# Kernel optimization log

Measured on AMD Instinct MI355X. Metric: run time of the kernel, lower is better.

## Reference

```python
import jax, jax.numpy as jnp
import numpy as np

DIM = 192
HEADS = 6
HEAD_DIM = DIM // HEADS
WS = 8            # window size
N = WS * WS       # tokens per window
IN_CC = 16        # top-k kept keys per query
B, H, W = 8, 64, 64
NEG = -100.0      # value used by the torch code for masked logits
EPS_NORM = 1e-12  # F.normalize eps
EPS_LN = 1e-5     # nn.LayerNorm eps


def _rel_pos_index(ws):
    coords = np.stack(np.meshgrid(np.arange(ws), np.arange(ws), indexing='ij'))  # (2,ws,ws)
    cf = coords.reshape(2, -1)
    rel = (cf[:, :, None] - cf[:, None, :]).transpose(1, 2, 0).astype(np.int64)  # (N,N,2)
    rel[:, :, 0] += ws - 1
    rel[:, :, 1] += ws - 1
    rel[:, :, 0] *= 2 * ws - 1
    return jnp.asarray(rel.sum(-1))  # (N,N) indices into (2ws-1)^2 table

REL_IDX = _rel_pos_index(WS)


def _layer_norm(x, g, b):
    mu = jnp.mean(x, -1, keepdims=True)
    var = jnp.mean(jnp.square(x - mu), -1, keepdims=True)
    return (x - mu) * jax.lax.rsqrt(var + EPS_LN) * g + b


def _l2n(x):
    n = jnp.sqrt(jnp.sum(jnp.square(x), -1, keepdims=True))
    return x / jnp.maximum(n, EPS_NORM)


def setup_inputs() -> dict:
    key = jax.random.key(0)
    ks = jax.random.split(key, 8)
    s = 0.02
    return {
        'x': jax.random.normal(ks[0], (B, DIM, H, W), jnp.float32),
        'norm1_g': jnp.ones((DIM,), jnp.float32),
        'norm1_b': jnp.zeros((DIM,), jnp.float32),
        'qkv_w': jax.random.normal(ks[1], (3 * DIM, DIM), jnp.float32) * s,
        'qkv_b': jnp.zeros((3 * DIM,), jnp.float32),
        'proj_w': jax.random.normal(ks[2], (DIM, DIM), jnp.float32) * s,
        'proj_b': jnp.zeros((DIM,), jnp.float32),
        'rpb_table': jax.random.normal(ks[3], ((2 * WS - 1) ** 2, HEADS), jnp.float32) * s,
        'temperature': jnp.ones((HEADS, 1, 1), jnp.float32),
        'norm2_g': jnp.ones((DIM,), jnp.float32),
        'norm2_b': jnp.zeros((DIM,), jnp.float32),
        'fc1_w': jax.random.normal(ks[4], (4 * DIM, DIM), jnp.float32) * s,
        'fc1_b': jnp.zeros((4 * DIM,), jnp.float32),
        'fc2_w': jax.random.normal(ks[5], (DIM, 4 * DIM), jnp.float32) * s,
        'fc2_b': jnp.zeros((DIM,), jnp.float32),
    }


def reference(x, norm1_g, norm1_b, qkv_w, qkv_b, proj_w, proj_b, rpb_table,
              temperature, norm2_g, norm2_b, fc1_w, fc1_b, fc2_w, fc2_b):
    b, c, h, w = x.shape
    # (B,C,H,W) -> (B,L,C), pre-norm (note: the torch code norms the shortcut too)
    xs = jnp.transpose(x.reshape(b, c, h * w), (0, 2, 1))
    shortcut = _layer_norm(xs, norm1_g, norm1_b)  # (B,L,C)

    # window partition: (B,H,W,C) -> (B*nWh*nWw, N, C); shift_size=0, no padding (H,W % WS == 0)
    xin = shortcut.reshape(b, h // WS, WS, w // WS, WS, c)
    xin = jnp.transpose(xin, (0, 1, 3, 2, 4, 5)).reshape(-1, N, c)
    B_ = xin.shape[0]

    qkv = (xin @ qkv_w.T + qkv_b).reshape(B_, N, 3, HEADS, HEAD_DIM)
    qkv = jnp.transpose(qkv, (2, 0, 3, 1, 4))  # (3, B_, h, N, d)
    q, k, v = qkv[0], qkv[1], qkv[2]

    # cosine attention with learned per-head temperature
    attn = jnp.einsum('bhnd,bhmd->bhnm', _l2n(q), _l2n(k)) * temperature  # (B_,h,N,N)

    # top-k sparsification: keep IN_CC largest logits per query (threshold == kth value;
    # equivalent to the torch topk+scatter mask for distinct values)
    kth = jax.lax.top_k(attn, IN_CC)[0][..., -1:]
    attn = jnp.where(attn >= kth, attn, NEG)

    # relative position bias gather: (N,N,h) -> (h,N,N)
    rpb = jnp.transpose(rpb_table[REL_IDX], (2, 0, 1))
    attn = jax.nn.softmax(attn + rpb[None], axis=-1)

    out = jnp.einsum('bhnm,bhmd->bhnd', attn, v)
    out = jnp.transpose(out, (0, 2, 1, 3)).reshape(B_, N, c)
    out = out @ proj_w.T + proj_b

    # window reverse -> (B, L, C)
    out = out.reshape(b, h // WS, w // WS, WS, WS, c)
    out = jnp.transpose(out, (0, 1, 3, 2, 4, 5)).reshape(b, h * w, c)

    x2 = shortcut + out  # drop_path = identity (eval)
    hdn = _layer_norm(x2, norm2_g, norm2_b)
    hdn = jax.nn.gelu(hdn @ fc1_w.T + fc1_b, approximate=False) @ fc2_w.T + fc2_b
    x2 = x2 + hdn

    # back to (B,C,H,W)
    return jnp.transpose(x2, (0, 2, 1)).reshape(b, c, h, w)
```

## Files before the change

kernel.cpp:

```cpp
#include <hip/hip_runtime.h>
#include <hip/hip_bf16.h>
#include <math.h>

#define DIM     192
#define HEADS   6
#define HEAD_DIM 32
#define NTOK    64
#define IN_CC   16
#define TTOT    32768
#define NWIN    512

using bf16x8 = __attribute__((ext_vector_type(8))) short;
using f32x4  = __attribute__((ext_vector_type(4))) float;
typedef unsigned short ushort_t;

__device__ __forceinline__ ushort_t f2b(float f) {
    unsigned u = __float_as_uint(f);
    u += 0x7fffu + ((u >> 16) & 1u);
    return (ushort_t)(u >> 16);
}
__device__ __forceinline__ unsigned pk2(float a, float b) {
    return (unsigned)f2b(a) | ((unsigned)f2b(b) << 16);
}
__device__ __forceinline__ float b2f(ushort_t u) {
    return __uint_as_float(((unsigned)u) << 16);
}

__global__ __launch_bounds__(256) void cvt_all_kernel(
    const float* __restrict__ s0, const float* __restrict__ s1,
    const float* __restrict__ s2, const float* __restrict__ s3,
    ushort_t* __restrict__ d0, ushort_t* __restrict__ d1,
    ushort_t* __restrict__ d2, ushort_t* __restrict__ d3)
{
    const int bid = blockIdx.x;
    const float* src; ushort_t* dst; int off, K; bool perm = false;
    if (bid < 108)      { src = s0; dst = d0; off = bid;       K = 192; perm = true; }
    else if (bid < 144) { src = s1; dst = d1; off = bid - 108; K = 192; }
    else if (bid < 288) { src = s2; dst = d2; off = bid - 144; K = 192; }
    else                { src = s3; dst = d3; off = bid - 288; K = 768; }
    const int K8 = K >> 3;
    const int d  = (off * 256 + threadIdx.x) * 4;
    const int frag = d >> 7, win = d & 127;
    const int m16w = win >> 3, k7 = win & 7;
    const int oblk = frag / K8, kblk = frag - oblk * K8;
    const int o = oblk * 16 + m16w, k = kblk * 8 + k7;
    int so = o;
    if (perm && o < 384) {
        const int s = o & 31;
        const int c = (((s >> 2) & 3) << 3) | (((s >> 4) & 1) << 2) | (s & 3);
        so = (o & ~31) | c;
    }
    float4 v = *(const float4*)(src + (size_t)so * K + k);
    ushort4 ov;
    ov.x = f2b(v.x); ov.y = f2b(v.y); ov.z = f2b(v.z); ov.w = f2b(v.w);
    *(ushort4*)(dst + d) = ov;
}

__global__ __launch_bounds__(256) void ln1_kernel(
    const float* __restrict__ x, const float* __restrict__ g,
    const float* __restrict__ bb, ushort_t* __restrict__ outh)
{
    __shared__ float xs[64][193];
    __shared__ float mu_s[64], rs_s[64];
    __shared__ float gs[192], bs[192];
    const int tid = threadIdx.x;
    const int t0  = blockIdx.x * 64;
    const int b   = t0 >> 12;
    const int hw0 = t0 & 4095;
    if (tid < 192) { gs[tid] = g[tid]; bs[tid] = bb[tid]; }
    const int tok = tid & 63, qq = tid >> 6;
    const float* xb = x + (size_t)b * (DIM * 4096) + hw0 + tok;
    #pragma unroll
    for (int it = 0; it < 48; ++it) {
        int c = it * 4 + qq;
        xs[tok][c] = xb[(size_t)c * 4096];
    }
    __syncthreads();
    const int tok2 = tid >> 2, p = tid & 3;
    float sum = 0.f;
    #pragma unroll
    for (int c = 0; c < 48; ++c) sum += xs[tok2][p * 48 + c];
    sum += __shfl_xor(sum, 1);
    sum += __shfl_xor(sum, 2);
    const float m = sum * (1.0f / 192.0f);
    float ss = 0.f;
    #pragma unroll
    for (int c = 0; c < 48; ++c) { float d = xs[tok2][p * 48 + c] - m; ss += d * d; }
    ss += __shfl_xor(ss, 1);
    ss += __shfl_xor(ss, 2);
    if (p == 0) {
        mu_s[tok2] = m;
        rs_s[tok2] = 1.0f / sqrtf(ss * (1.0f / 192.0f) + 1e-5f);
    }
    __syncthreads();
    ushort_t* obh = outh + (size_t)t0 * DIM;
    #pragma unroll
    for (int it = 0; it < 48; ++it) {
        int idx = it * 256 + tid;
        int tk = idx / 192, c = idx % 192;
        obh[idx] = f2b((xs[tk][c] - mu_s[tk]) * rs_s[tk] * gs[c] + bs[c]);
    }
}

__global__ __launch_bounds__(384, 3) void attn_fused(
    const ushort_t* __restrict__ sc_h, const ushort_t* __restrict__ wqf,
    const float* __restrict__ qkv_b, const float* __restrict__ rpb_table,
    const float* __restrict__ temp, const ushort_t* __restrict__ wpf,
    const float* __restrict__ proj_b, float* __restrict__ x2)
{
    __shared__ __align__(16) char smem[63840];
    const int tid  = threadIdx.x;
    const int wave = tid >> 6, n = tid & 63;
    char* arena = smem + wave * 9728;
    float*    Ssq = (float*)arena;
    ushort_t* Ph  = (ushort_t*)arena;
    ushort_t* Vt  = (ushort_t*)(arena + 4608);
    float*    ksb = (float*)(arena + 9216);
    float*    qnb = (float*)(arena + 9472);
    float*    rpb = (float*)(smem + 58368) + wave * 228;
    ushort_t (*AoT)[200] = (ushort_t(*)[200])smem;
    float* Cwj = (float*)(smem + 25600 + wave * 5120);

    const int win = blockIdx.x;
    const int h   = wave;
    const int b   = win >> 6;
    const int wh  = (win >> 3) & 7, ww = win & 7;
    const int i1  = n >> 3, j1 = n & 7;
    const int m16 = n & 15, quad = n >> 4;

    for (int r = n; r < 225; r += 64) rpb[r] = rpb_table[r * 6 + h];

    int trow[4];
    #pragma unroll
    for (int i = 0; i < 4; ++i) {
        const int row = 16 * i + m16;
        trow[i] = b * 4096 + (wh * 8 + (row >> 3)) * 64 + ww * 8 + (row & 7);
    }

    bf16x8 qA[4], kB[4];
    #pragma unroll
    for (int part = 0; part < 3; ++part) {
        const int o0 = part * 192 + h * 32;
        f32x4 pa[4][2];
        #pragma unroll
        for (int i = 0; i < 4; ++i)
            #pragma unroll
            for (int j = 0; j < 2; ++j)
                pa[i][j] = (f32x4)(0.0f);
        const ushort_t* Wb = wqf + (size_t)(o0 >> 4) * 24 * 128 + m16 * 8;
        for (int ks = 0; ks < 192; ks += 32) {
            bf16x8 af[4], wv[2];
            #pragma unroll
            for (int i = 0; i < 4; ++i)
                af[i] = *(const bf16x8*)(sc_h + (size_t)trow[i] * 192 + ks + quad * 8);
            #pragma unroll
            for (int j = 0; j < 2; ++j)
                wv[j] = *(const bf16x8*)(Wb + (size_t)(j * 24 + (ks >> 3) + quad) * 128);
            #pragma unroll
            for (int i = 0; i < 4; ++i)
                #pragma unroll
                for (int j = 0; j < 2; ++j)
                    pa[i][j] = __builtin_amdgcn_mfma_f32_16x16x32_bf16(wv[j], af[i], pa[i][j], 0, 0, 0);
        }
        if (part < 2) {
            const float4 bv0 = *(const float4*)&qkv_b[o0 + 8 * quad];
            const float4 bv1 = *(const float4*)&qkv_b[o0 + 8 * quad + 4];
            float ssq[4];
            #pragma unroll
            for (int i = 0; i < 4; ++i) {
                f32x4 v0 = pa[i][0], v1 = pa[i][1];
                v0[0] += bv0.x; v0[1] += bv0.y; v0[2] += bv0.z; v0[3] += bv0.w;
                v1[0] += bv1.x; v1[1] += bv1.y; v1[2] += bv1.z; v1[3] += bv1.w;
                float sq = 0.f;
                #pragma unroll
                for (int r = 0; r < 4; ++r) sq += v0[r] * v0[r] + v1[r] * v1[r];
                ssq[i] = sq;
                bf16x8 fr;
                fr[0] = (short)f2b(v0[0]); fr[1] = (short)f2b(v0[1]);
                fr[2] = (short)f2b(v0[2]); fr[3] = (short)f2b(v0[3]);
                fr[4] = (short)f2b(v1[0]); fr[5] = (short)f2b(v1[1]);
                fr[6] = (short)f2b(v1[2]); fr[7] = (short)f2b(v1[3]);
                if (part == 0) qA[i] = fr; else kB[i] = fr;
            }
            #pragma unroll
            for (int i = 0; i < 4; ++i) {
                ssq[i] += __shfl_xor(ssq[i], 16);
                ssq[i] += __shfl_xor(ssq[i], 32);
            }
            if (quad == 0) {
                #pragma unroll
                for (int i = 0; i < 4; ++i) {
                    if (part == 0) qnb[16 * i + m16] = ssq[i];
                    else           ksb[4 * m16 + i]  = 1.0f / fmaxf(sqrtf(ssq[i]), 1e-12f);
                }
            }
        } else {
            const float4 bv0 = *(const float4*)&qkv_b[o0 + quad * 4];
            const float4 bv1 = *(const float4*)&qkv_b[o0 + 16 + quad * 4];
            #pragma unroll
            for (int i = 0; i < 4; ++i) {
                f32x4 v0 = pa[i][0], v1 = pa[i][1];
                v0[0] += bv0.x; v0[1] += bv0.y; v0[2] += bv0.z; v0[3] += bv0.w;
                v1[0] += bv1.x; v1[1] += bv1.y; v1[2] += bv1.z; v1[3] += bv1.w;
                #pragma unroll
                for (int r = 0; r < 4; ++r) {
                    Vt[(quad * 4 + r) * 72 + 4 * m16 + i]      = f2b(v0[r]);
                    Vt[(16 + quad * 4 + r) * 72 + 4 * m16 + i] = f2b(v1[r]);
                }
            }
        }
    }

    f32x4 acc[4][4];
    #pragma unroll
    for (int i = 0; i < 4; ++i)
        #pragma unroll
        for (int j = 0; j < 4; ++j)
            acc[i][j] = __builtin_amdgcn_mfma_f32_16x16x32_bf16(qA[i], kB[j], (f32x4)(0.0f), 0, 0, 0);

    float s[64];
    #pragma unroll
    for (int i = 0; i < 4; ++i) {
        #pragma unroll
        for (int r = 0; r < 4; ++r) {
            f32x4 vv = { acc[i][0][r], acc[i][1][r], acc[i][2][r], acc[i][3][r] };
            *(f32x4*)&Ssq[(4 * quad + r) * 68 + 4 * m16] = vv;
        }
        if ((n >> 4) == i) {
            #pragma unroll
            for (int c = 0; c < 16; ++c)
                *(float4*)&s[4 * c] = *(const float4*)&Ssq[(n & 15) * 68 + 4 * c];
        }
    }

    const float qs = temp[h] / fmaxf(sqrtf(qnb[n]), 1e-12f);
    #pragma unroll
    for (int c = 0; c < 16; ++c) {
        float4 kv = *(const float4*)&ksb[4 * c];
        s[4*c+0] *= qs * kv.x; s[4*c+1] *= qs * kv.y;
        s[4*c+2] *= qs * kv.z; s[4*c+3] *= qs * kv.w;
    }

    float thr = 1e30f;
    for (int it = 0; it < IN_CC; ++it) {
        float mx = -1e30f;
        #pragma unroll
        for (int m = 0; m < 64; ++m) {
            float vv = (s[m] < thr) ? s[m] : -1e30f;
            mx = fmaxf(mx, vv);
        }
        thr = mx;
    }

    const int basen = i1 * 15 + j1;
    float mx = -1e30f;
    #pragma unroll
    for (int c = 0; c < 64; ++c) {
        const int m = 16 * (c & 3) + (c >> 2);
        const int i2 = m >> 3, j2 = m & 7;
        float vv = ((s[c] >= thr) ? s[c] : -100.0f)
                 + rpb[basen + (7 - i2) * 15 + (7 - j2)];
        s[c] = vv;
        mx = fmaxf(mx, vv);
    }
    float sum = 0.f;
    #pragma unroll
    for (int c = 0; c < 64; ++c) { float e = __expf(s[c] - mx); s[c] = e; sum += e; }
    const float inv = 1.0f / sum;
    #pragma unroll
    for (int c = 0; c < 64; ++c) s[c] *= inv;

    bf16x8 vb[2][2];
    #pragma unroll
    for (int kh2 = 0; kh2 < 2; ++kh2)
        #pragma unroll
        for (int j2 = 0; j2 < 2; ++j2)
            vb[kh2][j2] = *(const bf16x8*)&Vt[(16 * j2 + m16) * 72 + kh2 * 32 + quad * 8];

    f32x4 o[4][2];
    #pragma unroll
    for (int i = 0; i < 4; ++i)
        #pragma unroll
        for (int j2 = 0; j2 < 2; ++j2)
            o[i][j2] = (f32x4)(0.0f);
    #pragma unroll
    for (int hf = 0; hf < 2; ++hf) {
        if ((n >> 5) == hf) {
            #pragma unroll
            for (int g = 0; g < 8; ++g) {
                uint4 w;
                w.x = pk2(s[8*g+0], s[8*g+1]); w.y = pk2(s[8*g+2], s[8*g+3]);
                w.z = pk2(s[8*g+4], s[8*g+5]); w.w = pk2(s[8*g+6], s[8*g+7]);
                *(uint4*)&Ph[(n & 31) * 72 + 8 * g] = w;
            }
        }
        #pragma unroll
        for (int ih = 0; ih < 2; ++ih) {
            const int i = 2 * hf + ih;
            #pragma unroll
            for (int kh2 = 0; kh2 < 2; ++kh2) {
                bf16x8 pafr = *(const bf16x8*)&Ph[(16 * ih + m16) * 72 + kh2 * 32 + quad * 8];
                o[i][0] = __builtin_amdgcn_mfma_f32_16x16x32_bf16(pafr, vb[kh2][0], o[i][0], 0, 0, 0);
                o[i][1] = __builtin_amdgcn_mfma_f32_16x16x32_bf16(pafr, vb[kh2][1], o[i][1], 0, 0, 0);
            }
        }
    }
    __syncthreads();

    #pragma unroll
    for (int i = 0; i < 4; ++i) {
        #pragma unroll
        for (int r = 0; r < 4; ++r) {
            const int row = 16 * i + 4 * quad + r;
            AoT[row][h * 32 + m16]      = f2b(o[i][0][r]);
            AoT[row][h * 32 + 16 + m16] = f2b(o[i][1][r]);
        }
    }
    __syncthreads();

    f32x4 pacc[4][2];
    #pragma unroll
    for (int i = 0; i < 4; ++i)
        #pragma unroll
        for (int j = 0; j < 2; ++j)
            pacc[i][j] = (f32x4)(0.0f);
    const ushort_t* Wb = wpf + (size_t)(wave * 2) * 24 * 128 + m16 * 8;
    for (int ks = 0; ks < 192; ks += 32) {
        bf16x8 af[4], wv[2];
        #pragma unroll
        for (int i = 0; i < 4; ++i)
            af[i] = *(const bf16x8*)&AoT[16 * i + m16][quad * 8 + ks];
        #pragma unroll
        for (int j = 0; j < 2; ++j)
            wv[j] = *(const bf16x8*)(Wb + (size_t)(j * 24 + (ks >> 3) + quad) * 128);
        #pragma unroll
        for (int i = 0; i < 4; ++i)
            #pragma unroll
            for (int j = 0; j < 2; ++j)
                pacc[i][j] = __builtin_amdgcn_mfma_f32_16x16x32_bf16(wv[j], af[i], pacc[i][j], 0, 0, 0);
    }

    #pragma unroll
    for (int j = 0; j < 2; ++j) {
        const float4 bj = *(const float4*)&proj_b[wave * 32 + 16 * j + quad * 4];
        #pragma unroll
        for (int i = 0; i < 4; ++i) {
            f32x4 v = pacc[i][j];
            v[0] += bj.x; v[1] += bj.y; v[2] += bj.z; v[3] += bj.w;
            *(f32x4*)&Cwj[(16 * i + m16) * 20 + quad * 4] = v;
        }
        #pragma unroll
        for (int q = 0; q < 4; ++q) {
            const int idx = q * 64 + n;
            const int row = idx >> 2, c4 = (idx & 3) * 4;
            const int ii = row >> 3, jj = row & 7;
            const int tt = b * 4096 + (wh * 8 + ii) * 64 + ww * 8 + jj;
            const int oc = wave * 32 + 16 * j + c4;
            float4 vv = *(const float4*)&Cwj[row * 20 + c4];
            uint2 rv = *(const uint2*)&sc_h[(size_t)tt * 192 + oc];
            vv.x += b2f((ushort_t)(rv.x & 0xffffu));
            vv.y += b2f((ushort_t)(rv.x >> 16));
            vv.z += b2f((ushort_t)(rv.y & 0xffffu));
            vv.w += b2f((ushort_t)(rv.y >> 16));
            *(float4*)&x2[(size_t)tt * DIM + oc] = vv;
        }
    }
}

__global__ __launch_bounds__(256) void mlp_fused(
    const float* __restrict__ x2, const ushort_t* __restrict__ w1f,
    const ushort_t* __restrict__ w2f, const float* __restrict__ fc1_b,
    const float* __restrict__ fc2_b, const float* __restrict__ g2,
    const float* __restrict__ b2, float* __restrict__ outp)
{
    __shared__ __align__(16) char smem[43008];
    ushort_t (*h_h)[200] = (ushort_t(*)[200])smem;
    ushort_t (*a1c)[136] = (ushort_t(*)[136])(smem + 25600);
    float* gs  = (float*)(smem + 25600);
    float* bs  = gs + 192;

    const int tid  = threadIdx.x;
    const int wave = tid >> 6, lane = tid & 63;
    const int m16 = lane & 15, quad = lane >> 4;
    const int t0 = blockIdx.x * 64;
    const int b   = t0 >> 12;
    const int hw0 = t0 & 4095;

    if (tid < 192) { gs[tid] = g2[tid]; bs[tid] = b2[tid]; }
    __syncthreads();
    {
        const int tok = tid >> 2, p = tid & 3;
        const float* rp = x2 + (size_t)(t0 + tok) * DIM + p * 48;
        float xv[48];
        #pragma unroll
        for (int c4 = 0; c4 < 12; ++c4)
            *(float4*)&xv[c4 * 4] = *(const float4*)(rp + c4 * 4);
        float sum = 0.f;
        #pragma unroll
        for (int c = 0; c < 48; ++c) sum += xv[c];
        sum += __shfl_xor(sum, 1);
        sum += __shfl_xor(sum, 2);
        const float m = sum * (1.0f / 192.0f);
        float ss = 0.f;
        #pragma unroll
        for (int c = 0; c < 48; ++c) { float d = xv[c] - m; ss += d * d; }
        ss += __shfl_xor(ss, 1);
        ss += __shfl_xor(ss, 2);
        const float rs = 1.0f / sqrtf(ss * (1.0f / 192.0f) + 1e-5f);
        ushort_t* hp = &h_h[tok][p * 48];
        #pragma unroll
        for (int c2 = 0; c2 < 24; ++c2) {
            float v0 = (xv[2*c2]   - m) * rs * gs[p * 48 + 2*c2]   + bs[p * 48 + 2*c2];
            float v1 = (xv[2*c2+1] - m) * rs * gs[p * 48 + 2*c2+1] + bs[p * 48 + 2*c2+1];
            *(unsigned*)(hp + 2 * c2) = pk2(v0, v1);
        }
    }
    __syncthreads();

    f32x4 acc2[4][3];
    #pragma unroll
    for (int i = 0; i < 4; ++i)
        #pragma unroll
        for (int j = 0; j < 3; ++j)
            acc2[i][j] = (f32x4)(0.0f);

    for (int c = 0; c < 6; ++c) {
        f32x4 acc1[4][2];
        #pragma unroll
        for (int i = 0; i < 4; ++i)
            #pragma unroll
            for (int j = 0; j < 2; ++j)
                acc1[i][j] = (f32x4)(0.0f);
        const ushort_t* Wb1 = w1f + (size_t)(c * 8 + wave * 2) * 24 * 128 + m16 * 8;
        for (int ks = 0; ks < 192; ks += 32) {
            bf16x8 af[4], wv[2];
            #pragma unroll
            for (int i = 0; i < 4; ++i)
                af[i] = *(const bf16x8*)&h_h[16 * i + m16][quad * 8 + ks];
            #pragma unroll
            for (int j = 0; j < 2; ++j)
                wv[j] = *(const bf16x8*)(Wb1 + (size_t)(j * 24 + (ks >> 3) + quad) * 128);
            #pragma unroll
            for (int i = 0; i < 4; ++i)
                #pragma unroll
                for (int j = 0; j < 2; ++j)
                    acc1[i][j] = __builtin_amdgcn_mfma_f32_16x16x32_bf16(wv[j], af[i], acc1[i][j], 0, 0, 0);
        }
        #pragma unroll
        for (int j = 0; j < 2; ++j) {
            const int o = c * 128 + wave * 32 + 16 * j + quad * 4;
            const float4 bv = *(const float4*)&fc1_b[o];
            #pragma unroll
            for (int i = 0; i < 4; ++i) {
                f32x4 v = acc1[i][j];
                v[0] += bv.x; v[1] += bv.y; v[2] += bv.z; v[3] += bv.w;
                #pragma unroll
                for (int r = 0; r < 4; ++r) {
                    float xg = v[r];
                    float e1 = __expf(xg * (1.5957691f + 0.0713548f * xg * xg)) + 1.0f;
                    v[r] = xg - xg * __builtin_amdgcn_rcpf(e1);
                }
                uint2 pkd;
                pkd.x = pk2(v[0], v[1]); pkd.y = pk2(v[2], v[3]);
                *(uint2*)&a1c[16 * i + m16][wave * 32 + 16 * j + quad * 4] = pkd;
            }
        }
        __syncthreads();
        const ushort_t* Wb2 = w2f + (size_t)(wave * 3) * 96 * 128 + m16 * 8;
        for (int ks = 0; ks < 128; ks += 32) {
            bf16x8 af2[4], wv2[3];
            #pragma unroll
            for (int i = 0; i < 4; ++i)
                af2[i] = *(const bf16x8*)&a1c[16 * i + m16][quad * 8 + ks];
            #pragma unroll
            for (int j = 0; j < 3; ++j)
                wv2[j] = *(const bf16x8*)(Wb2 + (size_t)(j * 96 + c * 16 + (ks >> 3) + quad) * 128);
            #pragma unroll
            for (int i = 0; i < 4; ++i)
                #pragma unroll
                for (int j = 0; j < 3; ++j)
                    acc2[i][j] = __builtin_amdgcn_mfma_f32_16x16x32_bf16(wv2[j], af2[i], acc2[i][j], 0, 0, 0);
        }
        __syncthreads();
    }

    float (*Cw)[68] = (float(*)[68])(smem + wave * 8704);
    float4 b2j[3];
    #pragma unroll
    for (int j = 0; j < 3; ++j)
        b2j[j] = *(const float4*)&fc2_b[wave * 48 + 16 * j + quad * 4];
    #pragma unroll
    for (int p = 0; p < 2; ++p) {
        #pragma unroll
        for (int ih = 0; ih < 2; ++ih) {
            const int i = 2 * p + ih;
            #pragma unroll
            for (int j = 0; j < 3; ++j) {
                f32x4 v = acc2[i][j];
                v[0] += b2j[j].x; v[1] += b2j[j].y; v[2] += b2j[j].z; v[3] += b2j[j].w;
                *(f32x4*)&Cw[ih * 16 + m16][16 * j + quad * 4] = v;
            }
        }
        #pragma unroll
        for (int q = 0; q < 6; ++q) {
            const int idx = q * 64 + lane;
            const int cc = idx >> 3, t4 = (idx & 7) * 4;
            const int o  = wave * 48 + cc;
            const int tb = t0 + p * 32 + t4;
            float4 vv;
            vv.x = Cw[t4 + 0][cc] + x2[(size_t)(tb + 0) * DIM + o];
            vv.y = Cw[t4 + 1][cc] + x2[(size_t)(tb + 1) * DIM + o];
            vv.z = Cw[t4 + 2][cc] + x2[(size_t)(tb + 2) * DIM + o];
            vv.w = Cw[t4 + 3][cc] + x2[(size_t)(tb + 3) * DIM + o];
            *(float4*)&outp[(size_t)b * (DIM * 4096) + (size_t)o * 4096
                            + hw0 + p * 32 + t4] = vv;
        }
    }
}

extern "C" void kernel_launch(void* const* d_in, const int* in_sizes, int n_in,
                              void* d_out, int out_size, void* d_ws, size_t ws_size,
                              hipStream_t stream)
{
    const float* x        = (const float*)d_in[0];
    const float* norm1_g  = (const float*)d_in[1];
    const float* norm1_b  = (const float*)d_in[2];
    const float* qkv_w    = (const float*)d_in[3];
    const float* qkv_b    = (const float*)d_in[4];
    const float* proj_w   = (const float*)d_in[5];
    const float* proj_b   = (const float*)d_in[6];
    const float* rpbt     = (const float*)d_in[7];
    const float* temp     = (const float*)d_in[8];
    const float* norm2_g  = (const float*)d_in[9];
    const float* norm2_b  = (const float*)d_in[10];
    const float* fc1_w    = (const float*)d_in[11];
    const float* fc1_b    = (const float*)d_in[12];
    const float* fc2_w    = (const float*)d_in[13];
    const float* fc2_b    = (const float*)d_in[14];
    float* out = (float*)d_out;

    char* wsb = (char*)d_ws;
    ushort_t* shortcut_h = (ushort_t*)wsb;
    float*    x2         = (float*)(wsb + 12582912);
    ushort_t* wq  = (ushort_t*)(wsb + 125829120);
    ushort_t* wp  = wq + 110592;
    ushort_t* w1  = wp + 36864;
    ushort_t* w2  = w1 + 147456;

    hipLaunchKernelGGL(cvt_all_kernel, dim3(432), dim3(256), 0, stream,
                       qkv_w, proj_w, fc1_w, fc2_w, wq, wp, w1, w2);

    hipLaunchKernelGGL(ln1_kernel, dim3(TTOT / 64), dim3(256), 0, stream,
                       x, norm1_g, norm1_b, shortcut_h);
    hipLaunchKernelGGL(attn_fused, dim3(NWIN), dim3(384), 0, stream,
                       shortcut_h, wq, qkv_b, rpbt, temp, wp, proj_b, x2);
    hipLaunchKernelGGL(mlp_fused, dim3(TTOT / 64), dim3(256), 0, stream,
                       x2, w1, w2, fc1_b, fc2_b, norm2_g, norm2_b, out);
}
```

Before: 225.6 us.

## Process two windows per attention block and widen epilogue stores

The fused attention kernel now runs 12 waves per block, and each half of the block handles its own window. The grid is halved and shared memory is doubled, with separate AoT and per-wave scratch regions for each window. The projection epilogue is restructured so each lane writes 8 contiguous floats per row group, using 16-byte residual loads instead of the earlier 4-float scatter. The change keeps the same arithmetic. The risk is that launch_bounds(768,3) makes the compiler limit registers aggressively, which could cause spills, and larger blocks reduce scheduling flexibility.

Result: faster. 207.2 us (-8.1%).

```diff
diff --git a/kernel.cpp b/kernel.cpp
--- a/kernel.cpp
+++ b/kernel.cpp
@@ -102,13 +102,13 @@
     }
 }
 
-__global__ __launch_bounds__(384, 3) void attn_fused(
+__global__ __launch_bounds__(768, 3) void attn_fused(
     const ushort_t* __restrict__ sc_h, const ushort_t* __restrict__ wqf,
     const float* __restrict__ qkv_b, const float* __restrict__ rpb_table,
     const float* __restrict__ temp, const ushort_t* __restrict__ wpf,
     const float* __restrict__ proj_b, float* __restrict__ x2)
 {
-    __shared__ __align__(16) char smem[63840];
+    __shared__ __align__(16) char smem[127680];
     const int tid  = threadIdx.x;
     const int wave = tid >> 6, n = tid & 63;
     char* arena = smem + wave * 9728;
@@ -117,12 +117,14 @@
     ushort_t* Vt  = (ushort_t*)(arena + 4608);
     float*    ksb = (float*)(arena + 9216);
     float*    qnb = (float*)(arena + 9472);
-    float*    rpb = (float*)(smem + 58368) + wave * 228;
-    ushort_t (*AoT)[200] = (ushort_t(*)[200])smem;
-    float* Cwj = (float*)(smem + 25600 + wave * 5120);
-
-    const int win = blockIdx.x;
-    const int h   = wave;
+    float*    rpb = (float*)(smem + 116736) + wave * 228;
+
+    const int wloc = (wave >= 6) ? 1 : 0;
+    const int h    = wave - 6 * wloc;
+    ushort_t (*AoT)[200] = (ushort_t(*)[200])(smem + wloc * 25600);
+    float* Cwi = (float*)(smem + 51200 + wave * 2304);
+
+    const int win = blockIdx.x * 2 + wloc;
     const int b   = win >> 6;
     const int wh  = (win >> 3) & 7, ww = win & 7;
     const int i1  = n >> 3, j1 = n & 7;
@@ -324,7 +326,7 @@
         #pragma unroll
         for (int j = 0; j < 2; ++j)
             pacc[i][j] = (f32x4)(0.0f);
-    const ushort_t* Wb = wpf + (size_t)(wave * 2) * 24 * 128 + m16 * 8;
+    const ushort_t* Wb = wpf + (size_t)(h * 2) * 24 * 128 + m16 * 8;
     for (int ks = 0; ks < 192; ks += 32) {
         bf16x8 af[4], wv[2];
         #pragma unroll
@@ -340,30 +342,29 @@
                 pacc[i][j] = __builtin_amdgcn_mfma_f32_16x16x32_bf16(wv[j], af[i], pacc[i][j], 0, 0, 0);
     }
 
-    #pragma unroll
-    for (int j = 0; j < 2; ++j) {
-        const float4 bj = *(const float4*)&proj_b[wave * 32 + 16 * j + quad * 4];
-        #pragma unroll
-        for (int i = 0; i < 4; ++i) {
-            f32x4 v = pacc[i][j];
-            v[0] += bj.x; v[1] += bj.y; v[2] += bj.z; v[3] += bj.w;
-            *(f32x4*)&Cwj[(16 * i + m16) * 20 + quad * 4] = v;
-        }
-        #pragma unroll
-        for (int q = 0; q < 4; ++q) {
-            const int idx = q * 64 + n;
-            const int row = idx >> 2, c4 = (idx & 3) * 4;
-            const int ii = row >> 3, jj = row & 7;
-            const int tt = b * 4096 + (wh * 8 + ii) * 64 + ww * 8 + jj;
-            const int oc = wave * 32 + 16 * j + c4;
-            float4 vv = *(const float4*)&Cwj[row * 20 + c4];
-            uint2 rv = *(const uint2*)&sc_h[(size_t)tt * 192 + oc];
-            vv.x += b2f((ushort_t)(rv.x & 0xffffu));
-            vv.y += b2f((ushort_t)(rv.x >> 16));
-            vv.z += b2f((ushort_t)(rv.y & 0xffffu));
-            vv.w += b2f((ushort_t)(rv.y >> 16));
-            *(float4*)&x2[(size_t)tt * DIM + oc] = vv;
-        }
+    const float4 bj0 = *(const float4*)&proj_b[h * 32 + quad * 4];
+    const float4 bj1 = *(const float4*)&proj_b[h * 32 + 16 + quad * 4];
+    const int rr = n >> 2, ccc = n & 3;
+    #pragma unroll
+    for (int i = 0; i < 4; ++i) {
+        f32x4 v0 = pacc[i][0], v1 = pacc[i][1];
+        v0[0] += bj0.x; v0[1] += bj0.y; v0[2] += bj0.z; v0[3] += bj0.w;
+        v1[0] += bj1.x; v1[1] += bj1.y; v1[2] += bj1.z; v1[3] += bj1.w;
+        *(f32x4*)&Cwi[m16 * 36 + quad * 4]      = v0;
+        *(f32x4*)&Cwi[m16 * 36 + 16 + quad * 4] = v1;
+        const int tok = 16 * i + rr;
+        const int ii = tok >> 3, jj = tok & 7;
+        const int tt = b * 4096 + (wh * 8 + ii) * 64 + ww * 8 + jj;
+        const int oc = h * 32 + ccc * 8;
+        float4 w0 = *(const float4*)&Cwi[rr * 36 + ccc * 8];
+        float4 w1 = *(const float4*)&Cwi[rr * 36 + ccc * 8 + 4];
+        uint4 rv = *(const uint4*)&sc_h[(size_t)tt * 192 + oc];
+        w0.x += b2f((ushort_t)(rv.x & 0xffffu)); w0.y += b2f((ushort_t)(rv.x >> 16));
+        w0.z += b2f((ushort_t)(rv.y & 0xffffu)); w0.w += b2f((ushort_t)(rv.y >> 16));
+        w1.x += b2f((ushort_t)(rv.z & 0xffffu)); w1.y += b2f((ushort_t)(rv.z >> 16));
+        w1.z += b2f((ushort_t)(rv.w & 0xffffu)); w1.w += b2f((ushort_t)(rv.w >> 16));
+        *(float4*)&x2[(size_t)tt * DIM + oc]     = w0;
+        *(float4*)&x2[(size_t)tt * DIM + oc + 4] = w1;
     }
 }
 
@@ -552,7 +553,7 @@
 
     hipLaunchKernelGGL(ln1_kernel, dim3(TTOT / 64), dim3(256), 0, stream,
                        x, norm1_g, norm1_b, shortcut_h);
-    hipLaunchKernelGGL(attn_fused, dim3(NWIN), dim3(384), 0, stream,
+    hipLaunchKernelGGL(attn_fused, dim3(NWIN / 2), dim3(768), 0, stream,
                        shortcut_h, wq, qkv_b, rpbt, temp, wp, proj_b, x2);
     hipLaunchKernelGGL(mlp_fused, dim3(TTOT / 64), dim3(256), 0, stream,
                        x2, w1, w2, fc1_b, fc2_b, norm2_g, norm2_b, out);
```
